# Kernel optimization log

Measured on AMD Instinct MI355X. Metric: run time of the kernel, lower is better.

Reference implementation:

```python
import jax, jax.numpy as jnp
import numpy as np

DESIRED_SIZE = 512.0
STRIDE = DESIRED_SIZE / 16.0  # Constants.desired_size / 16
EPS = 1e-7
IOU_SCALE = 2.0
DIOU_SCALE = 0.5
SL1_SCALE = 1.0
GOOD_MULT = 2.0
BAD_MULT = 1.5


def setup_inputs() -> dict:
    key = jax.random.key(0)
    k1, k2 = jax.random.split(key)
    pred_boxes = jax.random.normal(k1, (64, 3, 32, 32, 5), dtype=jnp.float32)
    # uniform in [0, desired_size); every row has positive sum => all boxes valid,
    # so filter_and_trim keeps exactly max_boxes=100 per batch (fixed-k topk)
    target_boxes = jax.random.uniform(k2, (64, 100, 4), dtype=jnp.float32) * DESIRED_SIZE
    return {"pred_boxes": pred_boxes, "target_boxes": target_boxes}


def _postprocess(pred):
    # pred: [B, A, H, W, 5] -> absolute (x, y, w, h), conf
    B, A, H, W, _ = pred.shape
    cx = jnp.arange(W, dtype=pred.dtype)[None, None, None, :]
    cy = jnp.arange(H, dtype=pred.dtype)[None, None, :, None]
    x = (jax.nn.sigmoid(pred[..., 0]) + cx) * STRIDE
    y = (jax.nn.sigmoid(pred[..., 1]) + cy) * STRIDE
    wh = jnp.exp(pred[..., 2:4]) * STRIDE
    conf = jax.nn.sigmoid(pred[..., 4])
    return jnp.stack([x, y, wh[..., 0], wh[..., 1]], axis=-1), conf


def _fix_box_coordinates(b, epsilon=1.0):
    x1 = jnp.minimum(b[..., 0], b[..., 2])
    y1 = jnp.minimum(b[..., 1], b[..., 3])
    x2 = jnp.maximum(b[..., 0], b[..., 2])
    y2 = jnp.maximum(b[..., 1], b[..., 3])
    x2 = jnp.where(x1 == x2, x1 + epsilon, x2)
    y2 = jnp.where(y1 == y2, y1 + epsilon, y2)
    return jnp.stack([x1, y1, x2, y2], axis=-1)


def _yolo_to_corners(b):
    xc, yc, w, h = b[..., 0], b[..., 1], b[..., 2], b[..., 3]
    return jnp.stack([xc - w / 2, yc - h / 2, xc + w / 2, yc + h / 2], axis=-1)


def _box_iou(a, b):
    # torchvision.ops.box_iou: a [N,4], b [M,4] -> [N,M]
    area_a = (a[:, 2] - a[:, 0]) * (a[:, 3] - a[:, 1])
    area_b = (b[:, 2] - b[:, 0]) * (b[:, 3] - b[:, 1])
    lt = jnp.maximum(a[:, None, :2], b[None, :, :2])
    rb = jnp.minimum(a[:, None, 2:], b[None, :, 2:])
    wh = jnp.clip(rb - lt, 0.0)
    inter = wh[..., 0] * wh[..., 1]
    return inter / (area_a[:, None] + area_b[None, :] - inter)


def _diou_loss(p, t, eps=EPS):
    pa = jnp.clip(p[..., 2] - p[..., 0], 0.0) * jnp.clip(p[..., 3] - p[..., 1], 0.0)
    ta = jnp.clip(t[..., 2] - t[..., 0], 0.0) * jnp.clip(t[..., 3] - t[..., 1], 0.0)
    ix1 = jnp.maximum(p[..., 0], t[..., 0]); iy1 = jnp.maximum(p[..., 1], t[..., 1])
    ix2 = jnp.minimum(p[..., 2], t[..., 2]); iy2 = jnp.minimum(p[..., 3], t[..., 3])
    inter = jnp.clip(ix2 - ix1, 0.0) * jnp.clip(iy2 - iy1, 0.0)
    iou = inter / (pa + ta - inter + eps)
    pcx = (p[..., 0] + p[..., 2]) / 2; pcy = (p[..., 1] + p[..., 3]) / 2
    tcx = (t[..., 0] + t[..., 2]) / 2; tcy = (t[..., 1] + t[..., 3]) / 2
    cdist = (pcx - tcx) ** 2 + (pcy - tcy) ** 2
    ex1 = jnp.minimum(p[..., 0], t[..., 0]); ey1 = jnp.minimum(p[..., 1], t[..., 1])
    ex2 = jnp.maximum(p[..., 2], t[..., 2]); ey2 = jnp.maximum(p[..., 3], t[..., 3])
    diag = (ex2 - ex1) ** 2 + (ey2 - ey1) ** 2
    return 1.0 - (iou - cdist / (diag + eps))


def _smooth_l1_mean(p, t):
    d = p - t
    ad = jnp.abs(d)
    return jnp.mean(jnp.where(ad < 1.0, 0.5 * d * d, ad - 0.5))


def reference(pred_boxes, target_boxes):
    # negative-size penalty computed on RAW (pre-postprocess) width/height
    pw = pred_boxes[..., 2]
    ph = pred_boxes[..., 3]
    neg_pen = (jnp.clip(1.0 - pw, 0.0) + jnp.clip(1.0 - ph, 0.0)).mean()

    coords, conf = _postprocess(pred_boxes)
    B = pred_boxes.shape[0]
    coords = coords.reshape(B, -1, 4)   # [B, A*H*W, 4]
    conf = conf.reshape(B, -1)          # [B, A*H*W]

    K = target_boxes.shape[1]  # all targets valid by construction -> fixed k
    topv, topi = jax.lax.top_k(conf, K)                      # [B, K]
    pred_sel = jnp.take_along_axis(coords, topi[..., None], axis=1)  # [B, K, 4]

    target_flat = target_boxes.reshape(-1, 4)   # [N, 4], N = B*K
    pred_flat = pred_sel.reshape(-1, 4)
    conf_flat = topv.reshape(-1, 1)             # [N, 1]

    target_c = _fix_box_coordinates(target_flat)
    pred_c = _yolo_to_corners(pred_flat)

    # IoULoss: max over preds of full NxN IoU matrix, per target
    iou_mat = _box_iou(pred_c, target_c)
    max_iou = jnp.clip(jnp.nan_to_num(jnp.max(iou_mat, axis=0)), 0.0)
    iou_loss = 1.0 - max_iou                    # [N]

    sl1 = _smooth_l1_mean(pred_c, target_c) / DESIRED_SIZE  # scalar
    diou = _diou_loss(pred_c, target_c)         # [N]

    max_loss = IOU_SCALE + DIOU_SCALE + SL1_SCALE  # 3.5
    # NOTE: source adds UNSCALED diou into x (faithful to original)
    x = iou_loss * IOU_SCALE + diou + sl1 * SL1_SCALE   # [N]
    y = conf_flat                                        # [N, 1] -> broadcast to [N, N]
    good = jnp.sqrt((0.0 - x) ** 2 + (1.0 - y) ** 2) * GOOD_MULT
    bad = jnp.sqrt((max_loss - x) ** 2 + (1.0 - y) ** 2) * BAD_MULT
    losses = jnp.clip(jnp.mean(good - bad) + max_loss * BAD_MULT, 0.0)
    return losses + neg_pen
```

## Files before the change

### kernel.cpp

```cpp
#include <hip/hip_runtime.h>
#include <cmath>

#define NKEY 3072
#define KSEL 100
#define PCHUNK 200

static __device__ __forceinline__ float sigf(float v) {
    return 1.0f / (1.0f + expf(-v));
}

static __device__ double block_reduce_sum(double v) {
    __shared__ double sh[4];
    __syncthreads();
    for (int off = 32; off > 0; off >>= 1) v += __shfl_down(v, off, 64);
    int lane = threadIdx.x & 63, wid = threadIdx.x >> 6;
    if (lane == 0) sh[wid] = v;
    __syncthreads();
    v = (threadIdx.x < 4) ? sh[threadIdx.x] : 0.0;
    if (wid == 0) {
        v += __shfl_down(v, 2, 64);
        v += __shfl_down(v, 1, 64);
    }
    return v;
}

__global__ __launch_bounds__(256) void k_topk(const float* __restrict__ pred,
                                              const float* __restrict__ tgt,
                                              float* __restrict__ predc,
                                              float* __restrict__ targc,
                                              float* __restrict__ confv,
                                              unsigned int* __restrict__ maxiou_bits,
                                              double* __restrict__ negp ) {
    const int b = blockIdx.x;
    const int t = threadIdx.x;

    __shared__ unsigned long long keys[NKEY];
    __shared__ unsigned int hist[256];
    __shared__ unsigned long long sel[KSEL];
    __shared__ unsigned long long tkey_sh;
    __shared__ unsigned int scnt;
    __shared__ int bdigit_sh;
    __shared__ int bk_sh;

    if (t < KSEL) {
        int n = b * KSEL + t;
        const float* tb = tgt + (size_t)n * 4;
        float a0 = tb[0], a1 = tb[1], a2 = tb[2], a3 = tb[3];
        float x1 = fminf(a0, a2), y1 = fminf(a1, a3);
        float x2 = fmaxf(a0, a2), y2 = fmaxf(a1, a3);
        if (x1 == x2) x2 = x1 + 1.0f;
        if (y1 == y2) y2 = y1 + 1.0f;
        targc[n * 4 + 0] = x1; targc[n * 4 + 1] = y1;
        targc[n * 4 + 2] = x2; targc[n * 4 + 3] = y2;
        maxiou_bits[n] = 0u;
    }
    if (t == 0) scnt = 0;

    const float* pb = pred + (size_t)b * (NKEY * 5);
    float negacc = 0.0f;
    for (int r = 0; r < 12; ++r) {
        int idx = t + r * 256;
        const float* pe = pb + (size_t)idx * 5;
        float w = pe[2], h = pe[3], cl = pe[4];
        negacc += fmaxf(1.0f - w, 0.0f) + fmaxf(1.0f - h, 0.0f);
        float c = sigf(cl);
        keys[idx] = ((unsigned long long)__float_as_uint(c) << 32)
                  | (unsigned long long)(0xFFFFFFFFu - (unsigned)idx);
    }
    {
        double v = block_reduce_sum((double)negacc);
        if (t == 0) negp[b] = v;
    }
    __syncthreads();

    unsigned long long prefix = 0ull;
    int plen = 0;
    int k = KSEL;
    bool done = false;
    for (int round = 0; round < 8 && !done; ++round) {
        hist[t] = 0u;
        __syncthreads();
        int shift = 56 - 8 * round;
        for (int r = 0; r < 12; ++r) {
            unsigned long long key = keys[t + r * 256];
            if (plen == 0 || (key >> (64 - plen)) == (prefix >> (64 - plen))) {
                atomicAdd(&hist[(unsigned)((key >> shift) & 0xFFull)], 1u);
            }
        }
        __syncthreads();
        if (t < 64) {
            unsigned s0 = hist[4 * t + 0], s1 = hist[4 * t + 1];
            unsigned s2 = hist[4 * t + 2], s3 = hist[4 * t + 3];
            unsigned ssum = s0 + s1 + s2 + s3;
            unsigned suf = ssum;
            for (int off = 1; off < 64; off <<= 1) {
                unsigned o = __shfl_down(suf, off, 64);
                if (t + off < 64) suf += o;
            }
            unsigned above = suf - ssum;
            if (above < (unsigned)k && suf >= (unsigned)k) {
                unsigned hh[4] = {s0, s1, s2, s3};
                unsigned cum = above;
                for (int q = 3; q >= 0; --q) {
                    unsigned c = hh[q];
                    if (cum + c >= (unsigned)k) { bdigit_sh = 4 * t + q; bk_sh = k - (int)cum; break; }
                    cum += c;
                }
            }
        }
        __syncthreads();
        int d = bdigit_sh;
        k = bk_sh;
        prefix |= ((unsigned long long)(unsigned)d) << shift;
        plen += 8;
        unsigned ceq = hist[d];
        if (ceq == 1u) {
            for (int r = 0; r < 12; ++r) {
                unsigned long long key = keys[t + r * 256];
                if ((key >> (64 - plen)) == (prefix >> (64 - plen))) tkey_sh = key;
            }
            done = true;
        }
        __syncthreads();
    }
    unsigned long long T = tkey_sh;

    for (int r = 0; r < 12; ++r) {
        unsigned long long key = keys[t + r * 256];
        if (key >= T) {
            unsigned pos = atomicAdd(&scnt, 1u);
            sel[pos] = key;
        }
    }
    __syncthreads();
    if (t < KSEL) {
        unsigned long long key = sel[t];
        int rank = 0;
        for (int p = 0; p < KSEL; ++p) rank += (sel[p] > key) ? 1 : 0;
        unsigned idx = 0xFFFFFFFFu - (unsigned)(key & 0xFFFFFFFFull);
        float conf = __uint_as_float((unsigned)(key >> 32));
        int n = b * KSEL + rank;
        confv[n] = conf;
        const float* pe = pb + (size_t)idx * 5;
        int w = idx & 31, h = (idx >> 5) & 31;
        float x  = (sigf(pe[0]) + (float)w) * 32.0f;
        float y  = (sigf(pe[1]) + (float)h) * 32.0f;
        float bw = expf(pe[2]) * 32.0f;
        float bh = expf(pe[3]) * 32.0f;
        predc[n * 4 + 0] = x - bw * 0.5f;
        predc[n * 4 + 1] = y - bh * 0.5f;
        predc[n * 4 + 2] = x + bw * 0.5f;
        predc[n * 4 + 3] = y + bh * 0.5f;
    }
}

__global__ __launch_bounds__(256) void k_maxiou(const float* __restrict__ predc,
                                                const float* __restrict__ targc,
                                                unsigned int* __restrict__ maxiou_bits,
                                                float* __restrict__ diouv,
                                                double* __restrict__ sl1p ) {
    __shared__ float4 pl[PCHUNK];
    __shared__ float pa_sh[PCHUNK];
    int t = threadIdx.x;
    int j = blockIdx.x * 256 + t;
    const float4* pc4 = (const float4*)predc;
    int i0 = blockIdx.y * PCHUNK;
    for (int i = t; i < PCHUNK; i += 256) {
        float4 p = pc4[i0 + i];
        pl[i] = p;
        pa_sh[i] = (p.z - p.x) * (p.w - p.y);
    }
    float4 tj = ((const float4*)targc)[j];
    float ta = (tj.z - tj.x) * (tj.w - tj.y);
    __syncthreads();
    float m0 = 0.0f, m1 = 0.0f;
    #pragma unroll 2
    for (int i = 0; i < PCHUNK; i += 2) {
        float4 p = pl[i];
        float w0 = fmaxf(fminf(p.z, tj.z) - fmaxf(p.x, tj.x), 0.0f);
        float h0 = fmaxf(fminf(p.w, tj.w) - fmaxf(p.y, tj.y), 0.0f);
        float in0 = w0 * h0;
        float iou0 = in0 * __builtin_amdgcn_rcpf(pa_sh[i] + ta - in0);
        m0 = fmaxf(m0, iou0);
        float4 q = pl[i + 1];
        float w1 = fmaxf(fminf(q.z, tj.z) - fmaxf(q.x, tj.x), 0.0f);
        float h1 = fmaxf(fminf(q.w, tj.w) - fmaxf(q.y, tj.y), 0.0f);
        float in1 = w1 * h1;
        float iou1 = in1 * __builtin_amdgcn_rcpf(pa_sh[i + 1] + ta - in1);
        m1 = fmaxf(m1, iou1);
    }
    m0 = fmaxf(m0, m1);
    atomicMax(&maxiou_bits[j], __float_as_uint(m0));

    if (blockIdx.y == 0) {
        float4 p = pc4[j];
        float pa = fmaxf(p.z - p.x, 0.f) * fmaxf(p.w - p.y, 0.f);
        float ta2 = fmaxf(tj.z - tj.x, 0.f) * fmaxf(tj.w - tj.y, 0.f);
        float ix1 = fmaxf(p.x, tj.x), iy1 = fmaxf(p.y, tj.y);
        float ix2 = fminf(p.z, tj.z), iy2 = fminf(p.w, tj.w);
        float inter = fmaxf(ix2 - ix1, 0.f) * fmaxf(iy2 - iy1, 0.f);
        float iou = inter / (pa + ta2 - inter + 1e-7f);
        float pcx = (p.x + p.z) * 0.5f, pcy = (p.y + p.w) * 0.5f;
        float tcx = (tj.x + tj.z) * 0.5f, tcy = (tj.y + tj.w) * 0.5f;
        float cd = (pcx - tcx) * (pcx - tcx) + (pcy - tcy) * (pcy - tcy);
        float ex1 = fminf(p.x, tj.x), ey1 = fminf(p.y, tj.y);
        float ex2 = fmaxf(p.z, tj.z), ey2 = fmaxf(p.w, tj.w);
        float dg = (ex2 - ex1) * (ex2 - ex1) + (ey2 - ey1) * (ey2 - ey1);
        diouv[j] = 1.0f - (iou - cd / (dg + 1e-7f));
        double s = 0.0;
        {
            float d0 = p.x - tj.x, d1 = p.y - tj.y, d2 = p.z - tj.z, d3 = p.w - tj.w;
            float a0 = fabsf(d0), a1 = fabsf(d1), a2 = fabsf(d2), a3 = fabsf(d3);
            s += (double)(a0 < 1.f ? 0.5f * d0 * d0 : a0 - 0.5f);
            s += (double)(a1 < 1.f ? 0.5f * d1 * d1 : a1 - 0.5f);
            s += (double)(a2 < 1.f ? 0.5f * d2 * d2 : a2 - 0.5f);
            s += (double)(a3 < 1.f ? 0.5f * d3 * d3 : a3 - 0.5f);
        }
        double v = block_reduce_sum(s);
        if (t == 0) sl1p[blockIdx.x] = v;
    }
}

__global__ __launch_bounds__(256) void k_pair(const unsigned int* __restrict__ maxiou_bits,
                                              const float* __restrict__ diouv,
                                              const float* __restrict__ confv,
                                              const double* __restrict__ sl1p,
                                              double* __restrict__ pairp ) {
    __shared__ float oy2s[256];
    __shared__ float sl1_sh;
    int t = threadIdx.x;
    int j = blockIdx.x * 256 + t;
    if (t == 0) {
        double s = 0.0;
        for (int i = 0; i < 25; ++i) s += sl1p[i];
        sl1_sh = (float)(s / 25600.0 / 512.0);
    }
    {
        float oy = 1.0f - confv[blockIdx.y * 256 + t];
        oy2s[t] = oy * oy;
    }
    float mj = __uint_as_float(maxiou_bits[j]);
    float dj = diouv[j];
    __syncthreads();
    float xj = (1.0f - mj) * 2.0f + dj + sl1_sh;
    float a2 = xj * xj;
    float bb = 3.5f - xj;
    float b2 = bb * bb;
    float acc0 = 0.0f, acc1 = 0.0f;
    #pragma unroll 4
    for (int i = 0; i < 256; i += 2) {
        float o0 = oy2s[i], o1 = oy2s[i + 1];
        acc0 += 2.0f * __builtin_amdgcn_sqrtf(a2 + o0)
              - 1.5f * __builtin_amdgcn_sqrtf(b2 + o0);
        acc1 += 2.0f * __builtin_amdgcn_sqrtf(a2 + o1)
              - 1.5f * __builtin_amdgcn_sqrtf(b2 + o1);
    }
    double v = block_reduce_sum((double)(acc0 + acc1));
    if (t == 0) pairp[blockIdx.x * 25 + blockIdx.y] = v;
}

__global__ __launch_bounds__(256) void k_final(const double* __restrict__ pairp,
                                               const double* __restrict__ negp,
                                               float* __restrict__ out) {
    int t = threadIdx.x;
    double s = 0.0;
    for (int i = t; i < 625; i += 256) s += pairp[i];
    double ps = block_reduce_sum(s);
    double n = (t < 64) ? negp[t] : 0.0;
    double ns = block_reduce_sum(n);
    if (t == 0) {
        double mean_pair = ps / 40960000.0;
        float losses = fmaxf((float)mean_pair + 5.25f, 0.0f);
        float neg = (float)(ns / 196608.0);
        out[0] = losses + neg;
    }
}


extern "C" void kernel_launch(void* const* d_in, const int* in_sizes, int n_in,
                              void* d_out, int out_size, void* d_ws, size_t ws_size,
                              hipStream_t stream) {
    const float* pred = (const float*)d_in[0];
    const float* tgt  = (const float*)d_in[1];
    float* out = (float*)d_out;

    char* ws = (char*)d_ws;
    double* negp  = (double*)ws;
    double* sl1p  = negp + 64;
    double* pairp = negp + 96;
    float* fbase  = (float*)(ws + 6400);
    float* predc  = fbase;
    float* targc  = fbase + 25600;
    float* confv  = fbase + 51200;
    float* diouv  = fbase + 57600;
    unsigned int* maxiou_bits = (unsigned int*)(fbase + 64000);

    k_topk<<<64, 256, 0, stream>>>(pred, tgt, predc, targc, confv, maxiou_bits, negp);
    k_maxiou<<<dim3(25, 32), 256, 0, stream>>>(predc, targc, maxiou_bits, diouv, sl1p);
    k_pair<<<dim3(25, 25), 256, 0, stream>>>(maxiou_bits, diouv, confv, sl1p, pairp);
    k_final<<<1, 256, 0, stream>>>(pairp, negp, out);
}
```

Baseline: 107.8 us.

## Shrink topk to one wavefront, double maxiou grid, fuse final reduction into pair kernel

The top-k kernel now runs one 64-lane wavefront per batch, so its block reduction and several syncs become wave-level operations. The max-IoU kernel halves its prediction chunk and doubles the grid to add parallelism. The separate final kernel is removed: pair blocks atomically accumulate a double sum, and the last block to finish, found through an atomic counter, writes the output. This saves one launch but adds global atomics and a threadfence, and gives a fixed 64 threads per batch for the serial top-k work.

```diff
diff --git a/kernel.cpp b/kernel.cpp
--- a/kernel.cpp
+++ b/kernel.cpp
@@ -3,7 +3,7 @@
 
 #define NKEY 3072
 #define KSEL 100
-#define PCHUNK 200
+#define PCHUNK 100
 
 static __device__ __forceinline__ float sigf(float v) {
     return 1.0f / (1.0f + expf(-v));
@@ -24,13 +24,15 @@
     return v;
 }
 
-__global__ __launch_bounds__(256) void k_topk(const float* __restrict__ pred,
-                                              const float* __restrict__ tgt,
-                                              float* __restrict__ predc,
-                                              float* __restrict__ targc,
-                                              float* __restrict__ confv,
-                                              unsigned int* __restrict__ maxiou_bits,
-                                              double* __restrict__ negp ) {
+__global__ __launch_bounds__(64) void k_topk(const float* __restrict__ pred,
+                                             const float* __restrict__ tgt,
+                                             float* __restrict__ predc,
+                                             float* __restrict__ targc,
+                                             float* __restrict__ confv,
+                                             unsigned int* __restrict__ maxiou_bits,
+                                             double* __restrict__ negp ,
+                                             double* __restrict__ pair_sum,
+                                             unsigned int* __restrict__ done_cnt) {
     const int b = blockIdx.x;
     const int t = threadIdx.x;
 
@@ -42,8 +44,10 @@
     __shared__ int bdigit_sh;
     __shared__ int bk_sh;
 
-    if (t < KSEL) {
-        int n = b * KSEL + t;
+    if (b == 0 && t == 0) { *pair_sum = 0.0; *done_cnt = 0u; }
+
+    for (int n0 = t; n0 < KSEL; n0 += 64) {
+        int n = b * KSEL + n0;
         const float* tb = tgt + (size_t)n * 4;
         float a0 = tb[0], a1 = tb[1], a2 = tb[2], a3 = tb[3];
         float x1 = fminf(a0, a2), y1 = fminf(a1, a3);
@@ -57,18 +61,19 @@
     if (t == 0) scnt = 0;
 
     const float* pb = pred + (size_t)b * (NKEY * 5);
-    float negacc = 0.0f;
-    for (int r = 0; r < 12; ++r) {
-        int idx = t + r * 256;
+    double negacc = 0.0;
+    for (int r = 0; r < 48; ++r) {
+        int idx = t + r * 64;
         const float* pe = pb + (size_t)idx * 5;
         float w = pe[2], h = pe[3], cl = pe[4];
-        negacc += fmaxf(1.0f - w, 0.0f) + fmaxf(1.0f - h, 0.0f);
+        negacc += (double)(fmaxf(1.0f - w, 0.0f) + fmaxf(1.0f - h, 0.0f));
         float c = sigf(cl);
         keys[idx] = ((unsigned long long)__float_as_uint(c) << 32)
                   | (unsigned long long)(0xFFFFFFFFu - (unsigned)idx);
     }
     {
-        double v = block_reduce_sum((double)negacc);
+        double v = negacc;
+        for (int off = 32; off > 0; off >>= 1) v += __shfl_down(v, off, 64);
         if (t == 0) negp[b] = v;
     }
     __syncthreads();
@@ -78,17 +83,17 @@
     int k = KSEL;
     bool done = false;
     for (int round = 0; round < 8 && !done; ++round) {
-        hist[t] = 0u;
+        hist[t] = 0u; hist[t + 64] = 0u; hist[t + 128] = 0u; hist[t + 192] = 0u;
         __syncthreads();
         int shift = 56 - 8 * round;
-        for (int r = 0; r < 12; ++r) {
-            unsigned long long key = keys[t + r * 256];
+        for (int r = 0; r < 48; ++r) {
+            unsigned long long key = keys[t + r * 64];
             if (plen == 0 || (key >> (64 - plen)) == (prefix >> (64 - plen))) {
                 atomicAdd(&hist[(unsigned)((key >> shift) & 0xFFull)], 1u);
             }
         }
         __syncthreads();
-        if (t < 64) {
+        {
             unsigned s0 = hist[4 * t + 0], s1 = hist[4 * t + 1];
             unsigned s2 = hist[4 * t + 2], s3 = hist[4 * t + 3];
             unsigned ssum = s0 + s1 + s2 + s3;
@@ -115,8 +120,8 @@
         plen += 8;
         unsigned ceq = hist[d];
         if (ceq == 1u) {
-            for (int r = 0; r < 12; ++r) {
-                unsigned long long key = keys[t + r * 256];
+            for (int r = 0; r < 48; ++r) {
+                unsigned long long key = keys[t + r * 64];
                 if ((key >> (64 - plen)) == (prefix >> (64 - plen))) tkey_sh = key;
             }
             done = true;
@@ -125,16 +130,16 @@
     }
     unsigned long long T = tkey_sh;
 
-    for (int r = 0; r < 12; ++r) {
-        unsigned long long key = keys[t + r * 256];
+    for (int r = 0; r < 48; ++r) {
+        unsigned long long key = keys[t + r * 64];
         if (key >= T) {
             unsigned pos = atomicAdd(&scnt, 1u);
             sel[pos] = key;
         }
     }
     __syncthreads();
-    if (t < KSEL) {
-        unsigned long long key = sel[t];
+    for (int n0 = t; n0 < KSEL; n0 += 64) {
+        unsigned long long key = sel[n0];
         int rank = 0;
         for (int p = 0; p < KSEL; ++p) rank += (sel[p] > key) ? 1 : 0;
         unsigned idx = 0xFFFFFFFFu - (unsigned)(key & 0xFFFFFFFFull);
@@ -165,10 +170,10 @@
     int j = blockIdx.x * 256 + t;
     const float4* pc4 = (const float4*)predc;
     int i0 = blockIdx.y * PCHUNK;
-    for (int i = t; i < PCHUNK; i += 256) {
-        float4 p = pc4[i0 + i];
-        pl[i] = p;
-        pa_sh[i] = (p.z - p.x) * (p.w - p.y);
+    if (t < PCHUNK) {
+        float4 p = pc4[i0 + t];
+        pl[t] = p;
+        pa_sh[t] = (p.z - p.x) * (p.w - p.y);
     }
     float4 tj = ((const float4*)targc)[j];
     float ta = (tj.z - tj.x) * (tj.w - tj.y);
@@ -225,7 +230,10 @@
                                               const float* __restrict__ diouv,
                                               const float* __restrict__ confv,
                                               const double* __restrict__ sl1p,
-                                              double* __restrict__ pairp ) {
+                                              const double* __restrict__ negp,
+                                              double* __restrict__ pair_sum,
+                                              unsigned int* __restrict__ done_cnt,
+                                              float* __restrict__ out) {
     __shared__ float oy2s[256];
     __shared__ float sl1_sh;
     int t = threadIdx.x;
@@ -256,23 +264,19 @@
               - 1.5f * __builtin_amdgcn_sqrtf(b2 + o1);
     }
     double v = block_reduce_sum((double)(acc0 + acc1));
-    if (t == 0) pairp[blockIdx.x * 25 + blockIdx.y] = v;
-}
-
-__global__ __launch_bounds__(256) void k_final(const double* __restrict__ pairp,
-                                               const double* __restrict__ negp,
-                                               float* __restrict__ out) {
-    int t = threadIdx.x;
-    double s = 0.0;
-    for (int i = t; i < 625; i += 256) s += pairp[i];
-    double ps = block_reduce_sum(s);
-    double n = (t < 64) ? negp[t] : 0.0;
-    double ns = block_reduce_sum(n);
     if (t == 0) {
-        double mean_pair = ps / 40960000.0;
-        float losses = fmaxf((float)mean_pair + 5.25f, 0.0f);
-        float neg = (float)(ns / 196608.0);
-        out[0] = losses + neg;
+        atomicAdd(pair_sum, v);
+        __threadfence();
+        unsigned prev = atomicAdd(done_cnt, 1u);
+        if (prev == 624u) {
+            double ps = atomicAdd(pair_sum, 0.0);
+            double ns = 0.0;
+            for (int i = 0; i < 64; ++i) ns += negp[i];
+            double mean_pair = ps / 40960000.0;
+            float losses = fmaxf((float)mean_pair + 5.25f, 0.0f);
+            float neg = (float)(ns / 196608.0);
+            out[0] = losses + neg;
+        }
     }
 }
 
@@ -285,9 +289,10 @@
     float* out = (float*)d_out;
 
     char* ws = (char*)d_ws;
-    double* negp  = (double*)ws;
-    double* sl1p  = negp + 64;
-    double* pairp = negp + 96;
+    double* negp     = (double*)ws;
+    double* sl1p     = negp + 64;
+    double* pair_sum = negp + 96;
+    unsigned int* done_cnt = (unsigned int*)(negp + 97);
     float* fbase  = (float*)(ws + 6400);
     float* predc  = fbase;
     float* targc  = fbase + 25600;
@@ -295,8 +300,9 @@
     float* diouv  = fbase + 57600;
     unsigned int* maxiou_bits = (unsigned int*)(fbase + 64000);
 
-    k_topk<<<64, 256, 0, stream>>>(pred, tgt, predc, targc, confv, maxiou_bits, negp);
-    k_maxiou<<<dim3(25, 32), 256, 0, stream>>>(predc, targc, maxiou_bits, diouv, sl1p);
-    k_pair<<<dim3(25, 25), 256, 0, stream>>>(maxiou_bits, diouv, confv, sl1p, pairp);
-    k_final<<<1, 256, 0, stream>>>(pairp, negp, out);
-}
+    k_topk<<<64, 64, 0, stream>>>(pred, tgt, predc, targc, confv, maxiou_bits,
+                                  negp, pair_sum, done_cnt);
+    k_maxiou<<<dim3(25, 64), 256, 0, stream>>>(predc, targc, maxiou_bits, diouv, sl1p);
+    k_pair<<<dim3(25, 25), 256, 0, stream>>>(maxiou_bits, diouv, confv, sl1p,
+                                             negp, pair_sum, done_cnt, out);
+}
```

Measured after the change: 130.3 us. +20.8%, slower.

## Fuse DIoU/SL1 into topk kernel and final reduction into pair kernel

Applied to the files above, without the earlier changes.

Moves the per-pair DIoU and smooth-L1 computation out of the max-IoU kernel into the top-k kernel, using shared-memory copies of the selected predictions and targets. It also removes the separate final-reduction kernel: the pair kernel now atomically accumulates its partial sums, and the last block to finish, found with a done counter, writes the output. This saves one kernel launch and a serial tail. In exchange it adds double-precision atomics and a last-block pattern, and the summation order is no longer deterministic.

```diff
diff --git a/kernel.cpp b/kernel.cpp
--- a/kernel.cpp
+++ b/kernel.cpp
@@ -30,17 +30,25 @@
                                               float* __restrict__ targc,
                                               float* __restrict__ confv,
                                               unsigned int* __restrict__ maxiou_bits,
-                                              double* __restrict__ negp ) {
+                                              double* __restrict__ negp ,
+                                              float* __restrict__ diouv,
+                                              double* __restrict__ sl1p ,
+                                              double* __restrict__ pair_sum,
+                                              unsigned int* __restrict__ done_cnt) {
     const int b = blockIdx.x;
     const int t = threadIdx.x;
 
     __shared__ unsigned long long keys[NKEY];
     __shared__ unsigned int hist[256];
     __shared__ unsigned long long sel[KSEL];
+    __shared__ float4 pbox[KSEL];
+    __shared__ float4 tbox[KSEL];
     __shared__ unsigned long long tkey_sh;
     __shared__ unsigned int scnt;
     __shared__ int bdigit_sh;
     __shared__ int bk_sh;
+
+    if (b == 0 && t == 0) { *pair_sum = 0.0; *done_cnt = 0u; }
 
     if (t < KSEL) {
         int n = b * KSEL + t;
@@ -52,6 +60,7 @@
         if (y1 == y2) y2 = y1 + 1.0f;
         targc[n * 4 + 0] = x1; targc[n * 4 + 1] = y1;
         targc[n * 4 + 2] = x2; targc[n * 4 + 3] = y2;
+        tbox[t] = make_float4(x1, y1, x2, y2);
         maxiou_bits[n] = 0u;
     }
     if (t == 0) scnt = 0;
@@ -147,18 +156,45 @@
         float y  = (sigf(pe[1]) + (float)h) * 32.0f;
         float bw = expf(pe[2]) * 32.0f;
         float bh = expf(pe[3]) * 32.0f;
-        predc[n * 4 + 0] = x - bw * 0.5f;
-        predc[n * 4 + 1] = y - bh * 0.5f;
-        predc[n * 4 + 2] = x + bw * 0.5f;
-        predc[n * 4 + 3] = y + bh * 0.5f;
-    }
+        float4 pc = make_float4(x - bw * 0.5f, y - bh * 0.5f,
+                                x + bw * 0.5f, y + bh * 0.5f);
+        predc[n * 4 + 0] = pc.x; predc[n * 4 + 1] = pc.y;
+        predc[n * 4 + 2] = pc.z; predc[n * 4 + 3] = pc.w;
+        pbox[rank] = pc;
+    }
+    __syncthreads();
+
+    double s = 0.0;
+    if (t < KSEL) {
+        float4 p = pbox[t];
+        float4 tj = tbox[t];
+        float pa = fmaxf(p.z - p.x, 0.f) * fmaxf(p.w - p.y, 0.f);
+        float ta2 = fmaxf(tj.z - tj.x, 0.f) * fmaxf(tj.w - tj.y, 0.f);
+        float ix1 = fmaxf(p.x, tj.x), iy1 = fmaxf(p.y, tj.y);
+        float ix2 = fminf(p.z, tj.z), iy2 = fminf(p.w, tj.w);
+        float inter = fmaxf(ix2 - ix1, 0.f) * fmaxf(iy2 - iy1, 0.f);
+        float iou = inter / (pa + ta2 - inter + 1e-7f);
+        float pcx = (p.x + p.z) * 0.5f, pcy = (p.y + p.w) * 0.5f;
+        float tcx = (tj.x + tj.z) * 0.5f, tcy = (tj.y + tj.w) * 0.5f;
+        float cd = (pcx - tcx) * (pcx - tcx) + (pcy - tcy) * (pcy - tcy);
+        float ex1 = fminf(p.x, tj.x), ey1 = fminf(p.y, tj.y);
+        float ex2 = fmaxf(p.z, tj.z), ey2 = fmaxf(p.w, tj.w);
+        float dg = (ex2 - ex1) * (ex2 - ex1) + (ey2 - ey1) * (ey2 - ey1);
+        diouv[b * KSEL + t] = 1.0f - (iou - cd / (dg + 1e-7f));
+        float d0 = p.x - tj.x, d1 = p.y - tj.y, d2 = p.z - tj.z, d3 = p.w - tj.w;
+        float a0 = fabsf(d0), a1 = fabsf(d1), a2 = fabsf(d2), a3 = fabsf(d3);
+        s += (double)(a0 < 1.f ? 0.5f * d0 * d0 : a0 - 0.5f);
+        s += (double)(a1 < 1.f ? 0.5f * d1 * d1 : a1 - 0.5f);
+        s += (double)(a2 < 1.f ? 0.5f * d2 * d2 : a2 - 0.5f);
+        s += (double)(a3 < 1.f ? 0.5f * d3 * d3 : a3 - 0.5f);
+    }
+    double v = block_reduce_sum(s);
+    if (t == 0) sl1p[b] = v;
 }
 
 __global__ __launch_bounds__(256) void k_maxiou(const float* __restrict__ predc,
                                                 const float* __restrict__ targc,
-                                                unsigned int* __restrict__ maxiou_bits,
-                                                float* __restrict__ diouv,
-                                                double* __restrict__ sl1p ) {
+                                                unsigned int* __restrict__ maxiou_bits) {
     __shared__ float4 pl[PCHUNK];
     __shared__ float pa_sh[PCHUNK];
     int t = threadIdx.x;
@@ -191,48 +227,23 @@
     }
     m0 = fmaxf(m0, m1);
     atomicMax(&maxiou_bits[j], __float_as_uint(m0));
-
-    if (blockIdx.y == 0) {
-        float4 p = pc4[j];
-        float pa = fmaxf(p.z - p.x, 0.f) * fmaxf(p.w - p.y, 0.f);
-        float ta2 = fmaxf(tj.z - tj.x, 0.f) * fmaxf(tj.w - tj.y, 0.f);
-        float ix1 = fmaxf(p.x, tj.x), iy1 = fmaxf(p.y, tj.y);
-        float ix2 = fminf(p.z, tj.z), iy2 = fminf(p.w, tj.w);
-        float inter = fmaxf(ix2 - ix1, 0.f) * fmaxf(iy2 - iy1, 0.f);
-        float iou = inter / (pa + ta2 - inter + 1e-7f);
-        float pcx = (p.x + p.z) * 0.5f, pcy = (p.y + p.w) * 0.5f;
-        float tcx = (tj.x + tj.z) * 0.5f, tcy = (tj.y + tj.w) * 0.5f;
-        float cd = (pcx - tcx) * (pcx - tcx) + (pcy - tcy) * (pcy - tcy);
-        float ex1 = fminf(p.x, tj.x), ey1 = fminf(p.y, tj.y);
-        float ex2 = fmaxf(p.z, tj.z), ey2 = fmaxf(p.w, tj.w);
-        float dg = (ex2 - ex1) * (ex2 - ex1) + (ey2 - ey1) * (ey2 - ey1);
-        diouv[j] = 1.0f - (iou - cd / (dg + 1e-7f));
-        double s = 0.0;
-        {
-            float d0 = p.x - tj.x, d1 = p.y - tj.y, d2 = p.z - tj.z, d3 = p.w - tj.w;
-            float a0 = fabsf(d0), a1 = fabsf(d1), a2 = fabsf(d2), a3 = fabsf(d3);
-            s += (double)(a0 < 1.f ? 0.5f * d0 * d0 : a0 - 0.5f);
-            s += (double)(a1 < 1.f ? 0.5f * d1 * d1 : a1 - 0.5f);
-            s += (double)(a2 < 1.f ? 0.5f * d2 * d2 : a2 - 0.5f);
-            s += (double)(a3 < 1.f ? 0.5f * d3 * d3 : a3 - 0.5f);
-        }
-        double v = block_reduce_sum(s);
-        if (t == 0) sl1p[blockIdx.x] = v;
-    }
 }
 
 __global__ __launch_bounds__(256) void k_pair(const unsigned int* __restrict__ maxiou_bits,
                                               const float* __restrict__ diouv,
                                               const float* __restrict__ confv,
-                                              const double* __restrict__ sl1p,
-                                              double* __restrict__ pairp ) {
+                                              const double* __restrict__ sl1p ,
+                                              const double* __restrict__ negp,
+                                              double* __restrict__ pair_sum,
+                                              unsigned int* __restrict__ done_cnt,
+                                              float* __restrict__ out) {
     __shared__ float oy2s[256];
     __shared__ float sl1_sh;
     int t = threadIdx.x;
     int j = blockIdx.x * 256 + t;
     if (t == 0) {
         double s = 0.0;
-        for (int i = 0; i < 25; ++i) s += sl1p[i];
+        for (int i = 0; i < 64; ++i) s += sl1p[i];
         sl1_sh = (float)(s / 25600.0 / 512.0);
     }
     {
@@ -256,23 +267,19 @@
               - 1.5f * __builtin_amdgcn_sqrtf(b2 + o1);
     }
     double v = block_reduce_sum((double)(acc0 + acc1));
-    if (t == 0) pairp[blockIdx.x * 25 + blockIdx.y] = v;
-}
-
-__global__ __launch_bounds__(256) void k_final(const double* __restrict__ pairp,
-                                               const double* __restrict__ negp,
-                                               float* __restrict__ out) {
-    int t = threadIdx.x;
-    double s = 0.0;
-    for (int i = t; i < 625; i += 256) s += pairp[i];
-    double ps = block_reduce_sum(s);
-    double n = (t < 64) ? negp[t] : 0.0;
-    double ns = block_reduce_sum(n);
     if (t == 0) {
-        double mean_pair = ps / 40960000.0;
-        float losses = fmaxf((float)mean_pair + 5.25f, 0.0f);
-        float neg = (float)(ns / 196608.0);
-        out[0] = losses + neg;
+        atomicAdd(pair_sum, v);
+        __threadfence();
+        unsigned prev = atomicAdd(done_cnt, 1u);
+        if (prev == 624u) {
+            double ps = atomicAdd(pair_sum, 0.0);
+            double ns = 0.0;
+            for (int i = 0; i < 64; ++i) ns += negp[i];
+            double mean_pair = ps / 40960000.0;
+            float losses = fmaxf((float)mean_pair + 5.25f, 0.0f);
+            float neg = (float)(ns / 196608.0);
+            out[0] = losses + neg;
+        }
     }
 }
 
@@ -285,9 +292,10 @@
     float* out = (float*)d_out;
 
     char* ws = (char*)d_ws;
-    double* negp  = (double*)ws;
-    double* sl1p  = negp + 64;
-    double* pairp = negp + 96;
+    double* negp     = (double*)ws;
+    double* sl1p     = negp + 64;
+    double* pair_sum = negp + 128;
+    unsigned int* done_cnt = (unsigned int*)(negp + 129);
     float* fbase  = (float*)(ws + 6400);
     float* predc  = fbase;
     float* targc  = fbase + 25600;
@@ -295,8 +303,9 @@
     float* diouv  = fbase + 57600;
     unsigned int* maxiou_bits = (unsigned int*)(fbase + 64000);
 
-    k_topk<<<64, 256, 0, stream>>>(pred, tgt, predc, targc, confv, maxiou_bits, negp);
-    k_maxiou<<<dim3(25, 32), 256, 0, stream>>>(predc, targc, maxiou_bits, diouv, sl1p);
-    k_pair<<<dim3(25, 25), 256, 0, stream>>>(maxiou_bits, diouv, confv, sl1p, pairp);
-    k_final<<<1, 256, 0, stream>>>(pairp, negp, out);
-}
+    k_topk<<<64, 256, 0, stream>>>(pred, tgt, predc, targc, confv, maxiou_bits,
+                                   negp, diouv, sl1p, pair_sum, done_cnt);
+    k_maxiou<<<dim3(25, 32), 256, 0, stream>>>(predc, targc, maxiou_bits);
+    k_pair<<<dim3(25, 25), 256, 0, stream>>>(maxiou_bits, diouv, confv, sl1p,
+                                             negp, pair_sum, done_cnt, out);
+}
```

Result: slower. 115.8 us (+7.5%).
